# Kernel tuning notes

Measured on AMD Instinct MI355X. Metric: run time of the kernel, lower is better.

## Reference

```python
import jax, jax.numpy as jnp
import numpy as np

EPS = 1e-5  # BatchNorm eps
N_NODES, N_EDGES, F = 100000, 600000, 128


def setup_inputs() -> dict:
    key = jax.random.key(0)
    ks = jax.random.split(key, 16)
    inp = {
        "node_representations": jax.random.normal(ks[0], (N_NODES, F), jnp.float32),
        "edges": jax.random.randint(ks[1], (2, N_EDGES), 0, N_NODES, jnp.int64 if jax.config.jax_enable_x64 else jnp.int32),
        "edge_weights": jax.random.uniform(ks[2], (N_EDGES,), jnp.float32),
        # preprocess FFN: BatchNorm1d(F) [eval mode] + Linear(F, F) + GELU
        "pre_bn_gamma": jax.random.normal(ks[3], (F,), jnp.float32) * 0.1 + 1.0,
        "pre_bn_beta": jax.random.normal(ks[4], (F,), jnp.float32) * 0.1,
        "pre_bn_mean": jax.random.normal(ks[5], (F,), jnp.float32) * 0.1,
        "pre_bn_var": jax.random.uniform(ks[6], (F,), jnp.float32) * 0.5 + 0.5,
        "pre_w": jax.random.normal(ks[7], (F, F), jnp.float32) / np.sqrt(F),
        "pre_b": jnp.zeros((F,), jnp.float32),
        # update FFN: BatchNorm1d(2F) [eval mode] + Linear(2F, F) + GELU
        "upd_bn_gamma": jax.random.normal(ks[8], (2 * F,), jnp.float32) * 0.1 + 1.0,
        "upd_bn_beta": jax.random.normal(ks[9], (2 * F,), jnp.float32) * 0.1,
        "upd_bn_mean": jax.random.normal(ks[10], (2 * F,), jnp.float32) * 0.1,
        "upd_bn_var": jax.random.uniform(ks[11], (2 * F,), jnp.float32) * 0.5 + 0.5,
        "upd_w": jax.random.normal(ks[12], (2 * F, F), jnp.float32) / np.sqrt(2 * F),
        "upd_b": jnp.zeros((F,), jnp.float32),
    }
    return inp


def _bn_eval(x, gamma, beta, mean, var):
    return (x - mean) * (gamma / jnp.sqrt(var + EPS)) + beta


def reference(node_representations, edges, edge_weights,
              pre_bn_gamma, pre_bn_beta, pre_bn_mean, pre_bn_var, pre_w, pre_b,
              upd_bn_gamma, upd_bn_beta, upd_bn_mean, upd_bn_var, upd_w, upd_b):
    n_nodes, f = node_representations.shape
    node_idx, nbr_idx = edges[0], edges[1]
    # gather neighbour features: [E, F]
    x = node_representations[nbr_idx]
    # preprocess FFN (BN eval, dropout=identity in eval, linear, gelu)
    x = _bn_eval(x, pre_bn_gamma, pre_bn_beta, pre_bn_mean, pre_bn_var)
    x = jax.nn.gelu(x @ pre_w + pre_b, approximate=False)
    x = x * edge_weights[:, None]
    # mean aggregation (replicates torch.unique-on-expanded-indices counter = degree * F)
    agg = jax.ops.segment_sum(x, node_idx, num_segments=n_nodes)
    deg = jax.ops.segment_sum(jnp.ones_like(edge_weights), node_idx, num_segments=n_nodes)
    counter = (deg * f)[:, None]
    agg = jnp.where(counter > 0, agg / jnp.where(counter > 0, counter, 1.0), 0.0)
    # concat combine + update FFN
    emb = jnp.concatenate([node_representations, agg], axis=-1)
    emb = _bn_eval(emb, upd_bn_gamma, upd_bn_beta, upd_bn_mean, upd_bn_var)
    emb = jax.nn.gelu(emb @ upd_w + upd_b, approximate=False)
    return emb
```

## Files before the change

### kernel.cpp

```cpp
#include <hip/hip_runtime.h>
#include <math.h>

#define F 128
#define TWO_F 256
#define BN_EPS 1e-5f
#define PAD_A 136
#define PAD_A2 264
#define CSR_S 512

typedef unsigned short ushort_t;
typedef unsigned char uchar_t;
typedef __attribute__((ext_vector_type(8))) short bfrag;
typedef __attribute__((ext_vector_type(4))) float ffrag;
typedef __attribute__((ext_vector_type(2))) float floatx2;

__device__ __forceinline__ float gelu_exact(float x) {
    return 0.5f * x * (1.0f + erff(x * 0.70710678118654752f));
}
__device__ __forceinline__ ushort_t f2bf(float x) {
    unsigned int u = __float_as_uint(x);
    u = (u + 0x7FFFu + ((u >> 16) & 1u)) >> 16;
    return (ushort_t)u;
}
__device__ __forceinline__ unsigned int pk2(float a, float b) {
    return (unsigned int)f2bf(a) | ((unsigned int)f2bf(b) << 16);
}

__device__ __forceinline__ void fma4_fp8(float* acc, unsigned int d, float w) {
    floatx2 lo = __builtin_amdgcn_cvt_pk_f32_fp8(d, false);
    floatx2 hi = __builtin_amdgcn_cvt_pk_f32_fp8(d, true);
    acc[0] = fmaf(w, lo.x, acc[0]);
    acc[1] = fmaf(w, lo.y, acc[1]);
    acc[2] = fmaf(w, hi.x, acc[2]);
    acc[3] = fmaf(w, hi.y, acc[3]);
}
__device__ __forceinline__ void fma16_fp8(float* acc, uint4 a, float w) {
    fma4_fp8(acc + 0,  a.x, w); fma4_fp8(acc + 4,  a.y, w);
    fma4_fp8(acc + 8,  a.z, w); fma4_fp8(acc + 12, a.w, w);
}

template<bool OVF>
__device__ __forceinline__ void gather_edges(
    float* acc, const uchar_t* __restrict__ G8, const int2* __restrict__ csr_s,
    const int2* __restrict__ csr_g, int eBeg, int sIdx, int eIdx, int q) {
    int i = sIdx;
    while (i < eIdx) {
        int c = eIdx - i;
        c = (c > 8) ? 8 : c;
        uint4 av[8];
        float wv[8];
        #pragma unroll
        for (int j = 0; j < 8; ++j) {
            if (j < c) {
                int2 m = OVF ? csr_g[eBeg + i + j] : csr_s[i + j];
                wv[j] = __int_as_float(m.y);
                av[j] = *reinterpret_cast<const uint4*>(
                    G8 + (size_t)(unsigned int)m.x * F + q * 16);
            }
        }
        #pragma unroll
        for (int j = 0; j < 8; ++j)
            if (j < c) fma16_fp8(acc, av[j], wv[j]);
        i += c;
    }
}

__global__ __launch_bounds__(256) void prep(
    const float* __restrict__ pre_w, const float* __restrict__ pre_b,
    const float* __restrict__ g1, const float* __restrict__ be1,
    const float* __restrict__ m1, const float* __restrict__ v1,
    const float* __restrict__ upd_w, const float* __restrict__ upd_b,
    const float* __restrict__ g2, const float* __restrict__ be2,
    const float* __restrict__ m2, const float* __restrict__ v2,
    ushort_t* __restrict__ W1T, ushort_t* __restrict__ W2T,
    float* __restrict__ b1f, float* __restrict__ b2f,
    const int* __restrict__ edges, int* __restrict__ counts, int nEdges, int histBlocks) {
    const int t = threadIdx.x;
    if (blockIdx.x == 0) {
        __shared__ float t1[F], t2[TWO_F];
        if (t < F) {
            float s = g1[t] * rsqrtf(v1[t] + BN_EPS);
            t1[t] = be1[t] - m1[t] * s;
        }
        {
            float s = g2[t] * rsqrtf(v2[t] + BN_EPS);
            t2[t] = be2[t] - m2[t] * s;
        }
        __syncthreads();
        if (t < F) {
            float acc = pre_b[t];
            #pragma unroll 4
            for (int k = 0; k < F; ++k) acc = fmaf(t1[k], pre_w[k * F + t], acc);
            b1f[t] = acc;
        } else {
            int j = t - F;
            float acc = upd_b[j];
            #pragma unroll 4
            for (int k = 0; k < TWO_F; ++k) acc = fmaf(t2[k], upd_w[k * F + j], acc);
            b2f[j] = acc;
        }
    } else if (blockIdx.x <= 128) {
        int idx = (blockIdx.x - 1) * 256 + t;
        if (idx < F * F) {
            int k = idx & (F - 1), n = idx >> 7;
            float s = g1[k] * rsqrtf(v1[k] + BN_EPS);
            W1T[idx] = f2bf(s * pre_w[k * F + n]);
        }
        {
            int k = idx & (TWO_F - 1), n = idx >> 8;
            float s = g2[k] * rsqrtf(v2[k] + BN_EPS);
            W2T[idx] = f2bf(s * upd_w[k * F + n]);
        }
    } else {
        int b = blockIdx.x - 129;
        for (int i = b * 256 + t; i < nEdges; i += histBlocks * 256)
            atomicAdd(&counts[edges[i]], 1);
    }
}

__global__ __launch_bounds__(1024) void scan_pass1(const int* __restrict__ counts,
                                                   int* __restrict__ offsets,
                                                   int* __restrict__ blocksums, int n) {
    __shared__ int sb[1024];
    const int t = threadIdx.x;
    int idx = blockIdx.x * 1024 + t;
    int v = (idx < n) ? counts[idx] : 0;
    sb[t] = v;
    __syncthreads();
    for (int off = 1; off < 1024; off <<= 1) {
        int x = (t >= off) ? sb[t - off] : 0;
        __syncthreads();
        sb[t] += x;
        __syncthreads();
    }
    if (idx < n) offsets[idx + 1] = sb[t];
    if (t == 1023) blocksums[blockIdx.x] = sb[t];
}

__global__ __launch_bounds__(1024) void scan_pass3(const int* __restrict__ counts,
                                                   int* __restrict__ offsets,
                                                   const int* __restrict__ blocksums,
                                                   int* __restrict__ cursor, int n) {
    __shared__ int sb[1024];
    const int t = threadIdx.x;
    sb[t] = (t < blockIdx.x) ? blocksums[t] : 0;
    __syncthreads();
    #pragma unroll
    for (int off = 512; off > 0; off >>= 1) {
        if (t < off) sb[t] += sb[t + off];
        __syncthreads();
    }
    int base = sb[0];
    int idx = blockIdx.x * 1024 + t;
    if (idx < n) {
        int incl = offsets[idx + 1] + base;
        offsets[idx + 1] = incl;
        cursor[idx] = incl - counts[idx];
    }
    if (blockIdx.x == 0 && t == 0) offsets[0] = 0;
}

__global__ __launch_bounds__(256) void gemm1_fill(
    const float* __restrict__ nodes, const ushort_t* __restrict__ W1T,
    const float* __restrict__ b1f, uchar_t* __restrict__ G8, int nNodes,
    const int* __restrict__ edges, const float* __restrict__ ew,
    int* __restrict__ cursor, int2* __restrict__ csr, int nEdges,
    int gB, int fillBlocks) {
    __shared__ ushort_t As[64 * PAD_A];
    __shared__ float bs[F];
    const int t = threadIdx.x;

    if (blockIdx.x >= gB) {
        int b = blockIdx.x - gB;
        for (int e = b * 256 + t; e < nEdges; e += fillBlocks * 256) {
            int dst = edges[e];
            int pos = atomicAdd(&cursor[dst], 1);
            csr[pos] = make_int2(edges[nEdges + e], __float_as_int(ew[e]));
        }
        return;
    }

    const int base = blockIdx.x * 64;
    {
        int r = t >> 2, q = t & 3;
        int n = base + r;
        int sn = (n < nNodes) ? n : 0;
        const float4* src = reinterpret_cast<const float4*>(nodes + (size_t)sn * F + q * 32);
        uint4 pv[4];
        #pragma unroll
        for (int i = 0; i < 4; ++i) {
            float4 a = src[2 * i], b = src[2 * i + 1];
            pv[i].x = pk2(a.x, a.y); pv[i].y = pk2(a.z, a.w);
            pv[i].z = pk2(b.x, b.y); pv[i].w = pk2(b.z, b.w);
        }
        uint4* dst = reinterpret_cast<uint4*>(As + r * PAD_A + q * 32);
        #pragma unroll
        for (int i = 0; i < 4; ++i) dst[i] = pv[i];
    }
    if (t < F) bs[t] = b1f[t];
    __syncthreads();

    const int lane = t & 63, w = t >> 6;
    const int m = lane & 15, quad = lane >> 4;

    ffrag acc[8];
    #pragma unroll
    for (int c = 0; c < 8; ++c) acc[c] = (ffrag){0.f, 0.f, 0.f, 0.f};

    #pragma unroll
    for (int kk = 0; kk < 4; ++kk) {
        int k0 = kk * 32 + quad * 8;
        bfrag a = *reinterpret_cast<const bfrag*>(As + (w * 16 + m) * PAD_A + k0);
        #pragma unroll
        for (int c = 0; c < 8; ++c) {
            bfrag b = *reinterpret_cast<const bfrag*>(W1T + (size_t)(c * 16 + m) * F + k0);
            acc[c] = __builtin_amdgcn_mfma_f32_16x16x32_bf16(a, b, acc[c], 0, 0, 0);
        }
    }

    #pragma unroll
    for (int c = 0; c < 8; ++c) {
        int feat = c * 16 + m;
        float bj = bs[feat];
        #pragma unroll
        for (int i = 0; i < 4; ++i) {
            int n = base + w * 16 + quad * 4 + i;
            if (n < nNodes) {
                float v = gelu_exact(acc[c][i] + bj);
                int pkd = __builtin_amdgcn_cvt_pk_fp8_f32(v, v, 0, false);
                G8[(size_t)n * F + feat] = (uchar_t)(pkd & 0xFF);
            }
        }
    }
}

__global__ __launch_bounds__(256) void node_fused(
    const float* __restrict__ nodes, const uchar_t* __restrict__ G8,
    const int* __restrict__ offsets, const int2* __restrict__ csr,
    const ushort_t* __restrict__ W2T, const float* __restrict__ b2f,
    float* __restrict__ out, int nNodes) {
    __shared__ ushort_t As[32 * PAD_A2];
    __shared__ float bs[F];
    __shared__ int offs[33];
    __shared__ int2 csr_s[CSR_S];
    const int t = threadIdx.x;
    const int base = blockIdx.x * 32;
    const int r = t >> 3, q = t & 7;

    if (t < F) bs[t] = b2f[t];
    if (t < 33) {
        int idx = base + t;
        offs[t] = offsets[(idx < nNodes) ? idx : nNodes];
    }
    __syncthreads();

    const int eBeg = offs[0];
    const int nE = offs[32] - eBeg;
    const int nEc = (nE < CSR_S) ? nE : CSR_S;

    for (int i = t; i < nEc; i += 256) csr_s[i] = csr[eBeg + i];

    {
        int n = base + r;
        int sn = (n < nNodes) ? n : 0;
        const float4* src = reinterpret_cast<const float4*>(nodes + (size_t)sn * F + q * 16);
        uint4 pv[2];
        #pragma unroll
        for (int i = 0; i < 2; ++i) {
            float4 a = src[2 * i], b = src[2 * i + 1];
            pv[i].x = pk2(a.x, a.y); pv[i].y = pk2(a.z, a.w);
            pv[i].z = pk2(b.x, b.y); pv[i].w = pk2(b.z, b.w);
        }
        uint4* dst = reinterpret_cast<uint4*>(As + r * PAD_A2 + q * 16);
        dst[0] = pv[0]; dst[1] = pv[1];
    }
    __syncthreads();

    {
        float acc[16];
        #pragma unroll
        for (int j = 0; j < 16; ++j) acc[j] = 0.f;
        const int sIdx = offs[r] - eBeg;
        const int eIdx = offs[r + 1] - eBeg;
        if (eIdx <= nEc)
            gather_edges<false>(acc, G8, csr_s, csr, eBeg, sIdx, eIdx, q);
        else
            gather_edges<true>(acc, G8, csr_s, csr, eBeg, sIdx, eIdx, q);
        int deg = eIdx - sIdx;
        float inv = (deg > 0) ? 1.0f / ((float)deg * (float)F) : 0.f;
        unsigned int* dstu = reinterpret_cast<unsigned int*>(As + r * PAD_A2 + F + q * 16);
        #pragma unroll
        for (int j = 0; j < 8; ++j) dstu[j] = pk2(acc[2 * j] * inv, acc[2 * j + 1] * inv);
    }
    __syncthreads();

    const int lane = t & 63, w = t >> 6;
    const int m = lane & 15, quad = lane >> 4;
    const int rg = w & 1, cg = w >> 1;

    ffrag acc[4];
    #pragma unroll
    for (int c = 0; c < 4; ++c) acc[c] = (ffrag){0.f, 0.f, 0.f, 0.f};

    #pragma unroll
    for (int kk = 0; kk < 8; ++kk) {
        int k0 = kk * 32 + quad * 8;
        bfrag a = *reinterpret_cast<const bfrag*>(As + (rg * 16 + m) * PAD_A2 + k0);
        #pragma unroll
        for (int c = 0; c < 4; ++c) {
            int feat = cg * 64 + c * 16 + m;
            bfrag b = *reinterpret_cast<const bfrag*>(W2T + (size_t)feat * TWO_F + k0);
            acc[c] = __builtin_amdgcn_mfma_f32_16x16x32_bf16(a, b, acc[c], 0, 0, 0);
        }
    }

    #pragma unroll
    for (int c = 0; c < 4; ++c) {
        int feat = cg * 64 + c * 16 + m;
        float bj = bs[feat];
        #pragma unroll
        for (int i = 0; i < 4; ++i) {
            int n = base + rg * 16 + quad * 4 + i;
            if (n < nNodes) out[(size_t)n * F + feat] = gelu_exact(acc[c][i] + bj);
        }
    }
}

extern "C" void kernel_launch(void* const* d_in, const int* in_sizes, int n_in,
                              void* d_out, int out_size, void* d_ws, size_t ws_size,
                              hipStream_t stream) {
    const float* nodes  = (const float*)d_in[0];
    const int*   edges  = (const int*)d_in[1];
    const float* ew     = (const float*)d_in[2];
    const float* pre_g  = (const float*)d_in[3];
    const float* pre_be = (const float*)d_in[4];
    const float* pre_m  = (const float*)d_in[5];
    const float* pre_v  = (const float*)d_in[6];
    const float* pre_w  = (const float*)d_in[7];
    const float* pre_b  = (const float*)d_in[8];
    const float* upd_g  = (const float*)d_in[9];
    const float* upd_be = (const float*)d_in[10];
    const float* upd_m  = (const float*)d_in[11];
    const float* upd_v  = (const float*)d_in[12];
    const float* upd_w  = (const float*)d_in[13];
    const float* upd_b  = (const float*)d_in[14];
    float* out = (float*)d_out;

    const int nNodes = in_sizes[0] / F;
    const int nEdges = in_sizes[2];
    const int nChunks = (nNodes + 1023) / 1024;
    const int histBlocks = 1024;
    const int gB = (nNodes + 63) / 64;
    const int fillBlocks = 1024;

    char* p = (char*)d_ws;
    int*      counts    = (int*)p;       p += (size_t)nNodes * 4;
    int*      offsets   = (int*)p;       p += (size_t)(nNodes + 4) * 4;
    int*      cursor    = (int*)p;       p += (size_t)nNodes * 4;
    int*      blocksums = (int*)p;       p += 1024 * 4;
    int2*     csr       = (int2*)p;      p += (size_t)nEdges * 8;
    float*    b1f       = (float*)p;     p += F * 4;
    float*    b2f       = (float*)p;     p += F * 4;
    ushort_t* W1T       = (ushort_t*)p;  p += F * F * 2;
    ushort_t* W2T       = (ushort_t*)p;  p += TWO_F * F * 2;
    uchar_t*  G8        = (uchar_t*)p;

    hipMemsetAsync(counts, 0, (size_t)nNodes * 4, stream);

    prep<<<129 + histBlocks, 256, 0, stream>>>(
        pre_w, pre_b, pre_g, pre_be, pre_m, pre_v,
        upd_w, upd_b, upd_g, upd_be, upd_m, upd_v,
        W1T, W2T, b1f, b2f, edges, counts, nEdges, histBlocks);

    scan_pass1<<<nChunks, 1024, 0, stream>>>(counts, offsets, blocksums, nNodes);
    scan_pass3<<<nChunks, 1024, 0, stream>>>(counts, offsets, blocksums, cursor, nNodes);

    gemm1_fill<<<gB + fillBlocks, 256, 0, stream>>>(
        nodes, W1T, b1f, G8, nNodes, edges, ew, cursor, csr, nEdges, gB, fillBlocks);

    node_fused<<<(nNodes + 31) / 32, 256, 0, stream>>>(
        nodes, G8, offsets, csr, W2T, b2f, out, nNodes);
}
```

Before: 301.0 us.

## Split fused node kernel into separate gather-aggregate and GEMM kernels

Replaces the fused node kernel, which gathered neighbour features and then ran the update GEMM, with two kernels. The first writes bf16 mean-aggregated features to a workspace buffer, with no shared-memory CSR staging. The second stages the node and aggregate rows in LDS and runs the MFMA GEMM on 64-row tiles, each wave computing two 16-row fragments to reuse the weight fragments. This lets each phase run at its own occupancy and tile size, at the cost of an extra global write and read of the aggregate buffer and one more launch.

```diff
diff --git a/kernel.cpp b/kernel.cpp
--- a/kernel.cpp
+++ b/kernel.cpp
@@ -6,7 +6,6 @@
 #define BN_EPS 1e-5f
 #define PAD_A 136
 #define PAD_A2 264
-#define CSR_S 512
 
 typedef unsigned short ushort_t;
 typedef unsigned char uchar_t;
@@ -37,32 +36,6 @@
 __device__ __forceinline__ void fma16_fp8(float* acc, uint4 a, float w) {
     fma4_fp8(acc + 0,  a.x, w); fma4_fp8(acc + 4,  a.y, w);
     fma4_fp8(acc + 8,  a.z, w); fma4_fp8(acc + 12, a.w, w);
-}
-
-template<bool OVF>
-__device__ __forceinline__ void gather_edges(
-    float* acc, const uchar_t* __restrict__ G8, const int2* __restrict__ csr_s,
-    const int2* __restrict__ csr_g, int eBeg, int sIdx, int eIdx, int q) {
-    int i = sIdx;
-    while (i < eIdx) {
-        int c = eIdx - i;
-        c = (c > 8) ? 8 : c;
-        uint4 av[8];
-        float wv[8];
-        #pragma unroll
-        for (int j = 0; j < 8; ++j) {
-            if (j < c) {
-                int2 m = OVF ? csr_g[eBeg + i + j] : csr_s[i + j];
-                wv[j] = __int_as_float(m.y);
-                av[j] = *reinterpret_cast<const uint4*>(
-                    G8 + (size_t)(unsigned int)m.x * F + q * 16);
-            }
-        }
-        #pragma unroll
-        for (int j = 0; j < 8; ++j)
-            if (j < c) fma16_fp8(acc, av[j], wv[j]);
-        i += c;
-    }
 }
 
 __global__ __launch_bounds__(256) void prep(
@@ -234,83 +207,105 @@
     }
 }
 
-__global__ __launch_bounds__(256) void node_fused(
-    const float* __restrict__ nodes, const uchar_t* __restrict__ G8,
-    const int* __restrict__ offsets, const int2* __restrict__ csr,
+__global__ __launch_bounds__(256) void gather_agg(
+    const uchar_t* __restrict__ G8, const int* __restrict__ offsets,
+    const int2* __restrict__ csr, ushort_t* __restrict__ agg, int nNodes) {
+    const int t = threadIdx.x;
+    const int gid = blockIdx.x * 32 + (t >> 3);
+    const int q = t & 7;
+    if (gid >= nNodes) return;
+    const int s = offsets[gid], e = offsets[gid + 1];
+
+    float acc[16];
+    #pragma unroll
+    for (int j = 0; j < 16; ++j) acc[j] = 0.f;
+
+    int i = s;
+    while (i < e) {
+        int c = e - i;
+        c = (c > 8) ? 8 : c;
+        uint4 av[8];
+        float wv[8];
+        #pragma unroll
+        for (int j = 0; j < 8; ++j) {
+            if (j < c) {
+                int2 m = csr[i + j];
+                wv[j] = __int_as_float(m.y);
+                av[j] = *reinterpret_cast<const uint4*>(
+                    G8 + (size_t)(unsigned int)m.x * F + q * 16);
+            }
+        }
+        #pragma unroll
+        for (int j = 0; j < 8; ++j)
+            if (j < c) fma16_fp8(acc, av[j], wv[j]);
+        i += c;
+    }
+
+    const int deg = e - s;
+    const float inv = (deg > 0) ? 1.0f / ((float)deg * (float)F) : 0.f;
+    uint4 pv0, pv1;
+    pv0.x = pk2(acc[0] * inv, acc[1] * inv);  pv0.y = pk2(acc[2] * inv, acc[3] * inv);
+    pv0.z = pk2(acc[4] * inv, acc[5] * inv);  pv0.w = pk2(acc[6] * inv, acc[7] * inv);
+    pv1.x = pk2(acc[8] * inv, acc[9] * inv);  pv1.y = pk2(acc[10] * inv, acc[11] * inv);
+    pv1.z = pk2(acc[12] * inv, acc[13] * inv); pv1.w = pk2(acc[14] * inv, acc[15] * inv);
+    uint4* d = reinterpret_cast<uint4*>(agg + (size_t)gid * F + q * 16);
+    d[0] = pv0; d[1] = pv1;
+}
+
+__global__ __launch_bounds__(256) void gemm2(
+    const float* __restrict__ nodes, const ushort_t* __restrict__ agg,
     const ushort_t* __restrict__ W2T, const float* __restrict__ b2f,
     float* __restrict__ out, int nNodes) {
-    __shared__ ushort_t As[32 * PAD_A2];
+    __shared__ ushort_t As[64 * PAD_A2];
     __shared__ float bs[F];
-    __shared__ int offs[33];
-    __shared__ int2 csr_s[CSR_S];
-    const int t = threadIdx.x;
-    const int base = blockIdx.x * 32;
-    const int r = t >> 3, q = t & 7;
-
-    if (t < F) bs[t] = b2f[t];
-    if (t < 33) {
-        int idx = base + t;
-        offs[t] = offsets[(idx < nNodes) ? idx : nNodes];
-    }
-    __syncthreads();
-
-    const int eBeg = offs[0];
-    const int nE = offs[32] - eBeg;
-    const int nEc = (nE < CSR_S) ? nE : CSR_S;
-
-    for (int i = t; i < nEc; i += 256) csr_s[i] = csr[eBeg + i];
+    const int t = threadIdx.x;
+    const int base = blockIdx.x * 64;
 
     {
+        int r = t >> 2, q = t & 3;
         int n = base + r;
         int sn = (n < nNodes) ? n : 0;
-        const float4* src = reinterpret_cast<const float4*>(nodes + (size_t)sn * F + q * 16);
-        uint4 pv[2];
-        #pragma unroll
-        for (int i = 0; i < 2; ++i) {
+        const float4* src = reinterpret_cast<const float4*>(nodes + (size_t)sn * F + q * 32);
+        uint4 pv[4];
+        #pragma unroll
+        for (int i = 0; i < 4; ++i) {
             float4 a = src[2 * i], b = src[2 * i + 1];
             pv[i].x = pk2(a.x, a.y); pv[i].y = pk2(a.z, a.w);
             pv[i].z = pk2(b.x, b.y); pv[i].w = pk2(b.z, b.w);
         }
-        uint4* dst = reinterpret_cast<uint4*>(As + r * PAD_A2 + q * 16);
-        dst[0] = pv[0]; dst[1] = pv[1];
-    }
-    __syncthreads();
-
-    {
-        float acc[16];
-        #pragma unroll
-        for (int j = 0; j < 16; ++j) acc[j] = 0.f;
-        const int sIdx = offs[r] - eBeg;
-        const int eIdx = offs[r + 1] - eBeg;
-        if (eIdx <= nEc)
-            gather_edges<false>(acc, G8, csr_s, csr, eBeg, sIdx, eIdx, q);
-        else
-            gather_edges<true>(acc, G8, csr_s, csr, eBeg, sIdx, eIdx, q);
-        int deg = eIdx - sIdx;
-        float inv = (deg > 0) ? 1.0f / ((float)deg * (float)F) : 0.f;
-        unsigned int* dstu = reinterpret_cast<unsigned int*>(As + r * PAD_A2 + F + q * 16);
-        #pragma unroll
-        for (int j = 0; j < 8; ++j) dstu[j] = pk2(acc[2 * j] * inv, acc[2 * j + 1] * inv);
-    }
+        uint4* dst = reinterpret_cast<uint4*>(As + r * PAD_A2 + q * 32);
+        #pragma unroll
+        for (int i = 0; i < 4; ++i) dst[i] = pv[i];
+        const uint4* src2 = reinterpret_cast<const uint4*>(agg + (size_t)sn * F) + q * 4;
+        uint4* dst2 = reinterpret_cast<uint4*>(As + r * PAD_A2 + F + q * 32);
+        #pragma unroll
+        for (int i = 0; i < 4; ++i) dst2[i] = src2[i];
+    }
+    if (t < F) bs[t] = b2f[t];
     __syncthreads();
 
     const int lane = t & 63, w = t >> 6;
     const int m = lane & 15, quad = lane >> 4;
     const int rg = w & 1, cg = w >> 1;
 
-    ffrag acc[4];
-    #pragma unroll
-    for (int c = 0; c < 4; ++c) acc[c] = (ffrag){0.f, 0.f, 0.f, 0.f};
+    ffrag acc0[4], acc1[4];
+    #pragma unroll
+    for (int c = 0; c < 4; ++c) {
+        acc0[c] = (ffrag){0.f, 0.f, 0.f, 0.f};
+        acc1[c] = (ffrag){0.f, 0.f, 0.f, 0.f};
+    }
 
     #pragma unroll
     for (int kk = 0; kk < 8; ++kk) {
         int k0 = kk * 32 + quad * 8;
-        bfrag a = *reinterpret_cast<const bfrag*>(As + (rg * 16 + m) * PAD_A2 + k0);
+        bfrag a0 = *reinterpret_cast<const bfrag*>(As + (rg * 32 + m) * PAD_A2 + k0);
+        bfrag a1 = *reinterpret_cast<const bfrag*>(As + (rg * 32 + 16 + m) * PAD_A2 + k0);
         #pragma unroll
         for (int c = 0; c < 4; ++c) {
             int feat = cg * 64 + c * 16 + m;
             bfrag b = *reinterpret_cast<const bfrag*>(W2T + (size_t)feat * TWO_F + k0);
-            acc[c] = __builtin_amdgcn_mfma_f32_16x16x32_bf16(a, b, acc[c], 0, 0, 0);
+            acc0[c] = __builtin_amdgcn_mfma_f32_16x16x32_bf16(a0, b, acc0[c], 0, 0, 0);
+            acc1[c] = __builtin_amdgcn_mfma_f32_16x16x32_bf16(a1, b, acc1[c], 0, 0, 0);
         }
     }
 
@@ -320,8 +315,10 @@
         float bj = bs[feat];
         #pragma unroll
         for (int i = 0; i < 4; ++i) {
-            int n = base + rg * 16 + quad * 4 + i;
-            if (n < nNodes) out[(size_t)n * F + feat] = gelu_exact(acc[c][i] + bj);
+            int n0 = base + rg * 32 + quad * 4 + i;
+            if (n0 < nNodes) out[(size_t)n0 * F + feat] = gelu_exact(acc0[c][i] + bj);
+            int n1 = n0 + 16;
+            if (n1 < nNodes) out[(size_t)n1 * F + feat] = gelu_exact(acc1[c][i] + bj);
         }
     }
 }
@@ -363,7 +360,8 @@
     float*    b2f       = (float*)p;     p += F * 4;
     ushort_t* W1T       = (ushort_t*)p;  p += F * F * 2;
     ushort_t* W2T       = (ushort_t*)p;  p += TWO_F * F * 2;
-    uchar_t*  G8        = (uchar_t*)p;
+    uchar_t*  G8        = (uchar_t*)p;   p += (size_t)nNodes * F;
+    ushort_t* agg       = (ushort_t*)p;
 
     hipMemsetAsync(counts, 0, (size_t)nNodes * 4, stream);
 
@@ -378,6 +376,9 @@
     gemm1_fill<<<gB + fillBlocks, 256, 0, stream>>>(
         nodes, W1T, b1f, G8, nNodes, edges, ew, cursor, csr, nEdges, gB, fillBlocks);
 
-    node_fused<<<(nNodes + 31) / 32, 256, 0, stream>>>(
-        nodes, G8, offsets, csr, W2T, b2f, out, nNodes);
-}
+    gather_agg<<<(nNodes + 31) / 32, 256, 0, stream>>>(
+        G8, offsets, csr, agg, nNodes);
+
+    gemm2<<<(nNodes + 63) / 64, 256, 0, stream>>>(
+        nodes, agg, W2T, b2f, out, nNodes);
+}
```

After: 297.7 us. Within noise of the previous version (-1.1%).
